# Optimization experiments

Measured on AMD Instinct MI355X. Metric: run time of the kernel, lower is better.

## Reference

```python
import jax, jax.numpy as jnp
from jax import lax
import numpy as np

N_ITER = 50  # entmax.EntmaxBisect default n_iter


def _p(z, alpha):
    # inverse of g'(t) = t**(alpha-1): clamp then fractional power
    return jnp.maximum(z, 0.0) ** (1.0 / (alpha - 1.0))


def entmax_bisect(x, alpha):
    """alpha-entmax over the last axis via 50-step bisection (entmax.EntmaxBisect)."""
    am1 = alpha - 1.0
    X = x * am1
    d = X.shape[-1]
    max_val = jnp.max(X, axis=-1, keepdims=True)
    tau_lo = max_val - 1.0                    # max - _gp(1, alpha)
    tau_hi = max_val - (1.0 / d) ** am1       # max - _gp(1/d, alpha)
    f_lo = jnp.sum(_p(X - tau_lo, alpha), axis=-1, keepdims=True) - 1.0
    dm0 = tau_hi - tau_lo

    def body(i, carry):
        dm, tlo, _ = carry
        dm = dm / 2.0
        tau_m = tlo + dm
        p_m = _p(X - tau_m, alpha)
        f_m = jnp.sum(p_m, axis=-1, keepdims=True) - 1.0
        mask = (f_m * f_lo) >= 0.0
        tlo = jnp.where(mask, tau_m, tlo)
        return dm, tlo, p_m

    _, _, p_m = lax.fori_loop(0, N_ITER, body, (dm0, tau_lo, jnp.zeros_like(X)))
    # ensure_sum_one=True
    return p_m / jnp.sum(p_m, axis=-1, keepdims=True)


def setup_inputs() -> dict:
    key = jax.random.key(0)
    in_value = jax.random.normal(key, (2048, 32000), dtype=jnp.float32)
    alpha = jnp.asarray(1.5, dtype=jnp.float32)  # the q parameter
    return {"in_value": in_value, "alpha": alpha}


def reference(in_value, alpha):
    return entmax_bisect(in_value, alpha)
```

## Files before the change

### kernel.cpp

```cpp
#include <hip/hip_runtime.h>
#include <math.h>


#define D_DIM   32000
#define NV4     (D_DIM / 4)
#define BLOCK   512
#define NWAVE   (BLOCK / 64)
#define CAP     4096
#define NEWTON  26
#define NITER   50

__device__ __forceinline__ float wave_max(float v) {
#pragma unroll
    for (int off = 32; off > 0; off >>= 1) v = fmaxf(v, __shfl_xor(v, off, 64));
    return v;
}
__device__ __forceinline__ float wave_sum(float v) {
#pragma unroll
    for (int off = 32; off > 0; off >>= 1) v += __shfl_xor(v, off, 64);
    return v;
}
__device__ __forceinline__ float pf(float z, bool sq, float expo) {
    z = fmaxf(z, 0.0f);
    return sq ? z * z : powf(z, expo);
}

__global__ __launch_bounds__(BLOCK, 8)
void entmax_bisect_kernel(const float* __restrict__ x,
                          const float* __restrict__ alpha_p,
                          float* __restrict__ out) {
    const int row  = blockIdx.x;
    const int tid  = threadIdx.x;
    const int lane = tid & 63;
    const int wid  = tid >> 6;

    __shared__ float          s_val[CAP];
    __shared__ unsigned short s_idx[CAP];
    __shared__ float          s_red[NWAVE];
    __shared__ float          s_bc[2];
    __shared__ int            s_cnt;

    const float alpha = alpha_p[0];
    const float am1   = alpha - 1.0f;
    const float expo  = 1.0f / am1;
    const bool  sq    = (expo == 2.0f);

    const float4* __restrict__ x4 = (const float4*)(x + (size_t)row * D_DIM);
    float4*       __restrict__ o4 = (float4*)(out + (size_t)row * D_DIM);

    float mx = -INFINITY;
    for (int i4 = tid; i4 < NV4; i4 += BLOCK) {
        float4 v = x4[i4];
        mx = fmaxf(mx, fmaxf(fmaxf(v.x * am1, v.y * am1),
                             fmaxf(v.z * am1, v.w * am1)));
    }
    mx = wave_max(mx);
    if (lane == 0) s_red[wid] = mx;
    if (tid == 0) s_cnt = 0;
    __syncthreads();
    float max_val = s_red[0];
#pragma unroll
    for (int w = 1; w < NWAVE; ++w) max_val = fmaxf(max_val, s_red[w]);

    const float tau_lo0 = max_val - 1.0f;

    const float4 zero4 = make_float4(0.f, 0.f, 0.f, 0.f);
    for (int i4 = tid; i4 < NV4; i4 += BLOCK) {
        float4 v = x4[i4];
        float Xc[4] = {v.x * am1, v.y * am1, v.z * am1, v.w * am1};
        o4[i4] = zero4;
#pragma unroll
        for (int c = 0; c < 4; ++c) {
            const bool on = Xc[c] > tau_lo0;
            const unsigned long long m = __ballot(on);
            if (m) {
                const int leader = (int)__ffsll(m) - 1;
                int base = 0;
                if (lane == leader) base = atomicAdd(&s_cnt, (int)__popcll(m));
                base = __shfl(base, leader, 64);
                if (on) {
                    const int pos = base +
                        (int)__popcll(m & ((1ull << lane) - 1ull));
                    if (pos < CAP) {
                        s_val[pos] = Xc[c];
                        s_idx[pos] = (unsigned short)(i4 * 4 + c);
                    }
                }
            }
        }
    }
    __syncthreads();
    const int n_act = s_cnt;

    if (n_act <= CAP) {
        if (wid == 0) {
            float tau, S;
            if (sq) {
                tau = tau_lo0;
                for (int it = 0; it < NEWTON; ++it) {
                    float s1 = 0.f, s2 = 0.f;
                    for (int i = lane; i < n_act; i += 64) {
                        const float z = fmaxf(s_val[i] - tau, 0.f);
                        s1 += z; s2 += z * z;
                    }
#pragma unroll
                    for (int off = 32; off > 0; off >>= 1) {
                        s1 += __shfl_xor(s1, off, 64);
                        s2 += __shfl_xor(s2, off, 64);
                    }
                    tau += (s2 - 1.0f) / fmaxf(2.0f * s1, 1e-30f);
                }
                float s2 = 0.f;
                for (int i = lane; i < n_act; i += 64) {
                    const float z = fmaxf(s_val[i] - tau, 0.f);
                    s2 += z * z;
                }
                S = wave_sum(s2);
            } else {
                const float tau_hi = max_val - powf(1.0f / (float)D_DIM, am1);
                float dm = tau_hi - tau_lo0;
                float s = 0.f;
                for (int i = lane; i < n_act; i += 64)
                    s += pf(s_val[i] - tau_lo0, sq, expo);
                s = wave_sum(s);
                const float f_lo = s - 1.0f;
                float tlo = tau_lo0, tau_m = tau_lo0, fsum = s;
                for (int it = 0; it < NITER; ++it) {
                    dm *= 0.5f;
                    tau_m = tlo + dm;
                    float t = 0.f;
                    for (int i = lane; i < n_act; i += 64)
                        t += pf(s_val[i] - tau_m, sq, expo);
                    t = wave_sum(t);
                    fsum = t;
                    if ((t - 1.0f) * f_lo >= 0.0f) tlo = tau_m;
                }
                tau = tau_m; S = fsum;
            }
            if (lane == 0) { s_bc[0] = tau; s_bc[1] = S; }
        }
        __syncthreads();

        const float tau_f = s_bc[0];
        const float invS  = 1.0f / s_bc[1];
        for (int i = tid; i < n_act; i += BLOCK) {
            const float z = fmaxf(s_val[i] - tau_f, 0.f);
            const float p = sq ? z * z : powf(z, expo);
            out[(size_t)row * D_DIM + s_idx[i]] = p * invS;
        }
    } else {
        const float tau_hi = max_val - powf(1.0f / (float)D_DIM, am1);
        float dm = tau_hi - tau_lo0;
        float s = 0.f;
        for (int i4 = tid; i4 < NV4; i4 += BLOCK) {
            float4 v = x4[i4];
            s += pf(v.x * am1 - tau_lo0, sq, expo) + pf(v.y * am1 - tau_lo0, sq, expo)
               + pf(v.z * am1 - tau_lo0, sq, expo) + pf(v.w * am1 - tau_lo0, sq, expo);
        }
        s = wave_sum(s);
        __syncthreads();
        if (lane == 0) s_red[wid] = s;
        __syncthreads();
        float tot = 0.f;
#pragma unroll
        for (int w = 0; w < NWAVE; ++w) tot += s_red[w];
        const float f_lo = tot - 1.0f;
        float tlo = tau_lo0, tau_m = tau_lo0, fsum = tot;
        for (int it = 0; it < NITER; ++it) {
            dm *= 0.5f;
            tau_m = tlo + dm;
            float t = 0.f;
            for (int i4 = tid; i4 < NV4; i4 += BLOCK) {
                float4 v = x4[i4];
                t += pf(v.x * am1 - tau_m, sq, expo) + pf(v.y * am1 - tau_m, sq, expo)
                   + pf(v.z * am1 - tau_m, sq, expo) + pf(v.w * am1 - tau_m, sq, expo);
            }
            t = wave_sum(t);
            __syncthreads();
            if (lane == 0) s_red[wid] = t;
            __syncthreads();
            float tt = 0.f;
#pragma unroll
            for (int w = 0; w < NWAVE; ++w) tt += s_red[w];
            fsum = tt;
            if ((tt - 1.0f) * f_lo >= 0.0f) tlo = tau_m;
        }
        const float invS = 1.0f / fsum;
        __syncthreads();
        for (int i4 = tid; i4 < NV4; i4 += BLOCK) {
            float4 v = x4[i4];
            float4 o;
            o.x = pf(v.x * am1 - tau_m, sq, expo) * invS;
            o.y = pf(v.y * am1 - tau_m, sq, expo) * invS;
            o.z = pf(v.z * am1 - tau_m, sq, expo) * invS;
            o.w = pf(v.w * am1 - tau_m, sq, expo) * invS;
            o4[i4] = o;
        }
    }
}

extern "C" void kernel_launch(void* const* d_in, const int* in_sizes, int n_in,
                              void* d_out, int out_size, void* d_ws, size_t ws_size,
                              hipStream_t stream) {
    const float* x       = (const float*)d_in[0];
    const float* alpha_p = (const float*)d_in[1];
    float* out           = (float*)d_out;
    const int rows       = in_sizes[0] / D_DIM;
    entmax_bisect_kernel<<<rows, BLOCK, 0, stream>>>(x, alpha_p, out);
}
```

Baseline: 529.8 us.

## Fuse max pass into candidate collection using running shared atomic max

Merges the separate max-reduction pass and the candidate-collection pass into one sweep over the row. A running shared-memory maximum, kept as an order-preserving uint via atomicMax, filters candidates one iteration late, and the wave-ballot compaction becomes per-thread atomicAdd. Because the running max can only rise, early candidates are a superset of the true active set, so CAP grows to absorb the extra entries. Newton iteration now stops early once the step is tiny. This halves global reads of the input, at the cost of more shared atomics and a larger shared buffer that may lower occupancy.

```diff
diff --git a/kernel.cpp b/kernel.cpp
--- a/kernel.cpp
+++ b/kernel.cpp
@@ -6,15 +6,10 @@
 #define NV4     (D_DIM / 4)
 #define BLOCK   512
 #define NWAVE   (BLOCK / 64)
-#define CAP     4096
-#define NEWTON  26
+#define CAP     6144
+#define NEWTON_MAX 30
 #define NITER   50
 
-__device__ __forceinline__ float wave_max(float v) {
-#pragma unroll
-    for (int off = 32; off > 0; off >>= 1) v = fmaxf(v, __shfl_xor(v, off, 64));
-    return v;
-}
 __device__ __forceinline__ float wave_sum(float v) {
 #pragma unroll
     for (int off = 32; off > 0; off >>= 1) v += __shfl_xor(v, off, 64);
@@ -23,6 +18,13 @@
 __device__ __forceinline__ float pf(float z, bool sq, float expo) {
     z = fmaxf(z, 0.0f);
     return sq ? z * z : powf(z, expo);
+}
+__device__ __forceinline__ unsigned fflip(float f) {
+    unsigned u = __float_as_uint(f);
+    return u ^ ((u >> 31) ? 0xFFFFFFFFu : 0x80000000u);
+}
+__device__ __forceinline__ float funflip(unsigned u) {
+    return __uint_as_float(u ^ ((u & 0x80000000u) ? 0x80000000u : 0xFFFFFFFFu));
 }
 
 __global__ __launch_bounds__(BLOCK, 8)
@@ -39,6 +41,7 @@
     __shared__ float          s_red[NWAVE];
     __shared__ float          s_bc[2];
     __shared__ int            s_cnt;
+    volatile __shared__ unsigned s_gmax;
 
     const float alpha = alpha_p[0];
     const float am1   = alpha - 1.0f;
@@ -48,56 +51,74 @@
     const float4* __restrict__ x4 = (const float4*)(x + (size_t)row * D_DIM);
     float4*       __restrict__ o4 = (float4*)(out + (size_t)row * D_DIM);
 
-    float mx = -INFINITY;
+    if (tid == 0) { s_cnt = 0; s_gmax = 0u; }
+    __syncthreads();
+
+    const float4 zero4 = make_float4(0.f, 0.f, 0.f, 0.f);
+    float  pX[4];
+    int    pI4 = -1;
     for (int i4 = tid; i4 < NV4; i4 += BLOCK) {
         float4 v = x4[i4];
-        mx = fmaxf(mx, fmaxf(fmaxf(v.x * am1, v.y * am1),
-                             fmaxf(v.z * am1, v.w * am1)));
+        o4[i4] = zero4;
+        float X0 = v.x * am1, X1 = v.y * am1, X2 = v.z * am1, X3 = v.w * am1;
+        const float m4 = fmaxf(fmaxf(X0, X1), fmaxf(X2, X3));
+        const unsigned fm = fflip(m4);
+        if (fm > s_gmax) atomicMax((unsigned*)&s_gmax, fm);
+        if (pI4 >= 0) {
+            const float thr = funflip(s_gmax) - 1.0f;
+            const bool o0 = pX[0] > thr, o1 = pX[1] > thr,
+                       o2 = pX[2] > thr, o3 = pX[3] > thr;
+            const int cnt = (int)o0 + (int)o1 + (int)o2 + (int)o3;
+            if (cnt) {
+                int base = atomicAdd(&s_cnt, cnt);
+                const int bidx = pI4 * 4;
+#pragma unroll
+                for (int c = 0; c < 4; ++c) {
+                    const bool on = (c == 0) ? o0 : (c == 1) ? o1 : (c == 2) ? o2 : o3;
+                    if (on) {
+                        if (base < CAP) {
+                            s_val[base] = pX[c];
+                            s_idx[base] = (unsigned short)(bidx + c);
+                        }
+                        ++base;
+                    }
+                }
+            }
+        }
+        pX[0] = X0; pX[1] = X1; pX[2] = X2; pX[3] = X3; pI4 = i4;
     }
-    mx = wave_max(mx);
-    if (lane == 0) s_red[wid] = mx;
-    if (tid == 0) s_cnt = 0;
-    __syncthreads();
-    float max_val = s_red[0];
-#pragma unroll
-    for (int w = 1; w < NWAVE; ++w) max_val = fmaxf(max_val, s_red[w]);
-
-    const float tau_lo0 = max_val - 1.0f;
-
-    const float4 zero4 = make_float4(0.f, 0.f, 0.f, 0.f);
-    for (int i4 = tid; i4 < NV4; i4 += BLOCK) {
-        float4 v = x4[i4];
-        float Xc[4] = {v.x * am1, v.y * am1, v.z * am1, v.w * am1};
-        o4[i4] = zero4;
-#pragma unroll
-        for (int c = 0; c < 4; ++c) {
-            const bool on = Xc[c] > tau_lo0;
-            const unsigned long long m = __ballot(on);
-            if (m) {
-                const int leader = (int)__ffsll(m) - 1;
-                int base = 0;
-                if (lane == leader) base = atomicAdd(&s_cnt, (int)__popcll(m));
-                base = __shfl(base, leader, 64);
+    if (pI4 >= 0) {
+        const float thr = funflip(s_gmax) - 1.0f;
+        const bool o0 = pX[0] > thr, o1 = pX[1] > thr,
+                   o2 = pX[2] > thr, o3 = pX[3] > thr;
+        const int cnt = (int)o0 + (int)o1 + (int)o2 + (int)o3;
+        if (cnt) {
+            int base = atomicAdd(&s_cnt, cnt);
+            const int bidx = pI4 * 4;
+#pragma unroll
+            for (int c = 0; c < 4; ++c) {
+                const bool on = (c == 0) ? o0 : (c == 1) ? o1 : (c == 2) ? o2 : o3;
                 if (on) {
-                    const int pos = base +
-                        (int)__popcll(m & ((1ull << lane) - 1ull));
-                    if (pos < CAP) {
-                        s_val[pos] = Xc[c];
-                        s_idx[pos] = (unsigned short)(i4 * 4 + c);
-                    }
+                    if (base < CAP) {
+                        s_val[base] = pX[c];
+                        s_idx[base] = (unsigned short)(bidx + c);
+                    }
+                    ++base;
                 }
             }
         }
     }
     __syncthreads();
-    const int n_act = s_cnt;
+    const int   n_act   = s_cnt;
+    const float max_val = funflip(s_gmax);
+    const float tau_lo0 = max_val - 1.0f;
 
     if (n_act <= CAP) {
         if (wid == 0) {
             float tau, S;
             if (sq) {
                 tau = tau_lo0;
-                for (int it = 0; it < NEWTON; ++it) {
+                for (int it = 0; it < NEWTON_MAX; ++it) {
                     float s1 = 0.f, s2 = 0.f;
                     for (int i = lane; i < n_act; i += 64) {
                         const float z = fmaxf(s_val[i] - tau, 0.f);
@@ -108,7 +129,9 @@
                         s1 += __shfl_xor(s1, off, 64);
                         s2 += __shfl_xor(s2, off, 64);
                     }
-                    tau += (s2 - 1.0f) / fmaxf(2.0f * s1, 1e-30f);
+                    const float dtau = (s2 - 1.0f) / fmaxf(2.0f * s1, 1e-30f);
+                    tau += dtau;
+                    if (dtau < 1e-7f * fmaxf(1.0f, fabsf(tau))) break;
                 }
                 float s2 = 0.f;
                 for (int i = lane; i < n_act; i += 64) {
```

Result: faster. 488.8 us (-7.7%).

## Keep row in registers, compact per-thread, write output densely, early-exit Newton

Applied to the files above, without the earlier changes.

Loads each row once into a 64-float per-thread register array and reuses it for the max, the compaction, the fallback bisection and the final output. This replaces repeated global reads and the separate zero-fill plus scattered sparse writes. Compaction now does one atomicAdd per thread instead of per-wave ballots. Newton iterations stop early once the step is small. This raises register pressure (launch bounds lowered to 4 waves per EU), which reduces occupancy.

```diff
diff --git a/kernel.cpp b/kernel.cpp
--- a/kernel.cpp
+++ b/kernel.cpp
@@ -6,18 +6,20 @@
 #define NV4     (D_DIM / 4)
 #define BLOCK   512
 #define NWAVE   (BLOCK / 64)
-#define CAP     4096
-#define NEWTON  26
+#define KITER   16
+#define VPT     (4 * KITER)
+#define CAP     6144
+#define NEWTON_MAX 30
 #define NITER   50
 
+__device__ __forceinline__ float wave_sum(float v) {
+#pragma unroll
+    for (int off = 32; off > 0; off >>= 1) v += __shfl_xor(v, off, 64);
+    return v;
+}
 __device__ __forceinline__ float wave_max(float v) {
 #pragma unroll
     for (int off = 32; off > 0; off >>= 1) v = fmaxf(v, __shfl_xor(v, off, 64));
-    return v;
-}
-__device__ __forceinline__ float wave_sum(float v) {
-#pragma unroll
-    for (int off = 32; off > 0; off >>= 1) v += __shfl_xor(v, off, 64);
     return v;
 }
 __device__ __forceinline__ float pf(float z, bool sq, float expo) {
@@ -25,7 +27,7 @@
     return sq ? z * z : powf(z, expo);
 }
 
-__global__ __launch_bounds__(BLOCK, 8)
+__global__ __launch_bounds__(BLOCK, 4)
 void entmax_bisect_kernel(const float* __restrict__ x,
                           const float* __restrict__ alpha_p,
                           float* __restrict__ out) {
@@ -48,42 +50,52 @@
     const float4* __restrict__ x4 = (const float4*)(x + (size_t)row * D_DIM);
     float4*       __restrict__ o4 = (float4*)(out + (size_t)row * D_DIM);
 
-    float mx = -INFINITY;
-    for (int i4 = tid; i4 < NV4; i4 += BLOCK) {
-        float4 v = x4[i4];
-        mx = fmaxf(mx, fmaxf(fmaxf(v.x * am1, v.y * am1),
-                             fmaxf(v.z * am1, v.w * am1)));
+    if (tid == 0) s_cnt = 0;
+
+    float X[VPT];
+#pragma unroll
+    for (int k = 0; k < KITER; ++k) {
+        const int i4 = tid + k * BLOCK;
+        if (i4 < NV4) {
+            const float4 v = x4[i4];
+            X[4 * k + 0] = v.x * am1;
+            X[4 * k + 1] = v.y * am1;
+            X[4 * k + 2] = v.z * am1;
+            X[4 * k + 3] = v.w * am1;
+        } else {
+            X[4 * k + 0] = -INFINITY; X[4 * k + 1] = -INFINITY;
+            X[4 * k + 2] = -INFINITY; X[4 * k + 3] = -INFINITY;
+        }
     }
+
+    float mx = X[0];
+#pragma unroll
+    for (int j = 1; j < VPT; ++j) mx = fmaxf(mx, X[j]);
     mx = wave_max(mx);
     if (lane == 0) s_red[wid] = mx;
-    if (tid == 0) s_cnt = 0;
     __syncthreads();
     float max_val = s_red[0];
 #pragma unroll
     for (int w = 1; w < NWAVE; ++w) max_val = fmaxf(max_val, s_red[w]);
-
     const float tau_lo0 = max_val - 1.0f;
 
-    const float4 zero4 = make_float4(0.f, 0.f, 0.f, 0.f);
-    for (int i4 = tid; i4 < NV4; i4 += BLOCK) {
-        float4 v = x4[i4];
-        float Xc[4] = {v.x * am1, v.y * am1, v.z * am1, v.w * am1};
-        o4[i4] = zero4;
-#pragma unroll
-        for (int c = 0; c < 4; ++c) {
-            const bool on = Xc[c] > tau_lo0;
-            const unsigned long long m = __ballot(on);
-            if (m) {
-                const int leader = (int)__ffsll(m) - 1;
-                int base = 0;
-                if (lane == leader) base = atomicAdd(&s_cnt, (int)__popcll(m));
-                base = __shfl(base, leader, 64);
-                if (on) {
-                    const int pos = base +
-                        (int)__popcll(m & ((1ull << lane) - 1ull));
-                    if (pos < CAP) {
-                        s_val[pos] = Xc[c];
-                        s_idx[pos] = (unsigned short)(i4 * 4 + c);
+    {
+        int cnt = 0;
+#pragma unroll
+        for (int j = 0; j < VPT; ++j) cnt += (int)(X[j] > tau_lo0);
+        if (cnt) {
+            int base = atomicAdd(&s_cnt, cnt);
+#pragma unroll
+            for (int k = 0; k < KITER; ++k) {
+#pragma unroll
+                for (int c = 0; c < 4; ++c) {
+                    const float xv = X[4 * k + c];
+                    if (xv > tau_lo0) {
+                        if (base < CAP) {
+                            s_val[base] = xv;
+                            s_idx[base] = (unsigned short)((tid + k * BLOCK) * 4 + c);
+                        }
+                        ++base;
                     }
                 }
             }
@@ -97,7 +109,7 @@
             float tau, S;
             if (sq) {
                 tau = tau_lo0;
-                for (int it = 0; it < NEWTON; ++it) {
+                for (int it = 0; it < NEWTON_MAX; ++it) {
                     float s1 = 0.f, s2 = 0.f;
                     for (int i = lane; i < n_act; i += 64) {
                         const float z = fmaxf(s_val[i] - tau, 0.f);
@@ -108,7 +120,9 @@
                         s1 += __shfl_xor(s1, off, 64);
                         s2 += __shfl_xor(s2, off, 64);
                     }
-                    tau += (s2 - 1.0f) / fmaxf(2.0f * s1, 1e-30f);
+                    const float dtau = (s2 - 1.0f) / fmaxf(2.0f * s1, 1e-30f);
+                    tau += dtau;
+                    if (dtau < 1e-7f * fmaxf(1.0f, fabsf(tau))) break;
                 }
                 float s2 = 0.f;
                 for (int i = lane; i < n_act; i += 64) {
@@ -143,22 +157,25 @@
 
         const float tau_f = s_bc[0];
         const float invS  = 1.0f / s_bc[1];
-        for (int i = tid; i < n_act; i += BLOCK) {
-            const float z = fmaxf(s_val[i] - tau_f, 0.f);
-            const float p = sq ? z * z : powf(z, expo);
-            out[(size_t)row * D_DIM + s_idx[i]] = p * invS;
+#pragma unroll
+        for (int k = 0; k < KITER; ++k) {
+            const int i4 = tid + k * BLOCK;
+            if (i4 < NV4) {
+                float4 o;
+                o.x = pf(X[4 * k + 0] - tau_f, sq, expo) * invS;
+                o.y = pf(X[4 * k + 1] - tau_f, sq, expo) * invS;
+                o.z = pf(X[4 * k + 2] - tau_f, sq, expo) * invS;
+                o.w = pf(X[4 * k + 3] - tau_f, sq, expo) * invS;
+                o4[i4] = o;
+            }
         }
     } else {
         const float tau_hi = max_val - powf(1.0f / (float)D_DIM, am1);
         float dm = tau_hi - tau_lo0;
         float s = 0.f;
-        for (int i4 = tid; i4 < NV4; i4 += BLOCK) {
-            float4 v = x4[i4];
-            s += pf(v.x * am1 - tau_lo0, sq, expo) + pf(v.y * am1 - tau_lo0, sq, expo)
-               + pf(v.z * am1 - tau_lo0, sq, expo) + pf(v.w * am1 - tau_lo0, sq, expo);
-        }
+#pragma unroll
+        for (int j = 0; j < VPT; ++j) s += pf(X[j] - tau_lo0, sq, expo);
         s = wave_sum(s);
-        __syncthreads();
         if (lane == 0) s_red[wid] = s;
         __syncthreads();
         float tot = 0.f;
@@ -170,11 +187,8 @@
             dm *= 0.5f;
             tau_m = tlo + dm;
             float t = 0.f;
-            for (int i4 = tid; i4 < NV4; i4 += BLOCK) {
-                float4 v = x4[i4];
-                t += pf(v.x * am1 - tau_m, sq, expo) + pf(v.y * am1 - tau_m, sq, expo)
-                   + pf(v.z * am1 - tau_m, sq, expo) + pf(v.w * am1 - tau_m, sq, expo);
-            }
+#pragma unroll
+            for (int j = 0; j < VPT; ++j) t += pf(X[j] - tau_m, sq, expo);
             t = wave_sum(t);
             __syncthreads();
             if (lane == 0) s_red[wid] = t;
@@ -186,15 +200,17 @@
             if ((tt - 1.0f) * f_lo >= 0.0f) tlo = tau_m;
         }
         const float invS = 1.0f / fsum;
-        __syncthreads();
-        for (int i4 = tid; i4 < NV4; i4 += BLOCK) {
-            float4 v = x4[i4];
-            float4 o;
-            o.x = pf(v.x * am1 - tau_m, sq, expo) * invS;
-            o.y = pf(v.y * am1 - tau_m, sq, expo) * invS;
-            o.z = pf(v.z * am1 - tau_m, sq, expo) * invS;
-            o.w = pf(v.w * am1 - tau_m, sq, expo) * invS;
-            o4[i4] = o;
+#pragma unroll
+        for (int k = 0; k < KITER; ++k) {
+            const int i4 = tid + k * BLOCK;
+            if (i4 < NV4) {
+                float4 o;
+                o.x = pf(X[4 * k + 0] - tau_m, sq, expo) * invS;
+                o.y = pf(X[4 * k + 1] - tau_m, sq, expo) * invS;
+                o.z = pf(X[4 * k + 2] - tau_m, sq, expo) * invS;
+                o.w = pf(X[4 * k + 3] - tau_m, sq, expo) * invS;
+                o4[i4] = o;
+            }
         }
     }
 }
```

After: 662.1 us. 1.25x slower.
